# Performance work log

Hardware: AMD Instinct MI355X
Metric: run time of the kernel (lower is better)

The kernel has to match this reference:

```python
import jax, jax.numpy as jnp
import numpy as np
import math

B, T, D = 2, 2048, 1024
H, HD = 16, 64  # n_heads, head_dim; H*HD == D

def setup_inputs() -> dict:
    key = jax.random.key(0)
    ks = jax.random.split(key, 5)
    s = 1.0 / math.sqrt(D)
    return {
        "x": jax.random.normal(ks[0], (B, T, D), dtype=jnp.float32),
        "w_qkv": jax.random.normal(ks[1], (D, 3 * D), dtype=jnp.float32) * s,
        "b_qkv": jax.random.normal(ks[2], (3 * D,), dtype=jnp.float32) * 0.01,
        "w_o": jax.random.normal(ks[3], (D, D), dtype=jnp.float32) * s,
        "b_o": jax.random.normal(ks[4], (D,), dtype=jnp.float32) * 0.01,
    }

def reference(x, w_qkv, b_qkv, w_o, b_o):
    b, t, d_model = x.shape
    qkv = x @ w_qkv + b_qkv                       # [b,t,3d]
    q, k, v = jnp.split(qkv, 3, axis=-1)
    # [b,t,d] -> [b,h,t,hd]
    q = q.reshape(b, t, H, HD).transpose(0, 2, 1, 3)
    k = k.reshape(b, t, H, HD).transpose(0, 2, 1, 3)
    v = v.reshape(b, t, H, HD).transpose(0, 2, 1, 3)
    # NOTE: original scales by sqrt(d_model), not sqrt(head_dim)
    scores = jnp.einsum('bhqd,bhkd->bhqk', q, k) / math.sqrt(d_model)
    causal = jnp.tril(jnp.ones((t, t), dtype=bool))
    scores = jnp.where(causal[None, None], scores, -jnp.inf)
    # dropout p=0.0 (pre-softmax in original) is identity
    attn = jax.nn.softmax(scores, axis=-1)
    y = jnp.einsum('bhqk,bhkd->bhqd', attn, v)    # [b,h,t,hd]
    y = y.transpose(0, 2, 1, 3).reshape(b, t, d_model)
    return y @ w_o + b_o
```

## Files before the change

### kernel.cpp

```cpp
#include <hip/hip_runtime.h>
#include <math.h>

typedef __bf16 bf16;
typedef __bf16 bf16x4 __attribute__((ext_vector_type(4)));
typedef __bf16 bf16x8 __attribute__((ext_vector_type(8)));
typedef float f32x4 __attribute__((ext_vector_type(4)));

__device__ __forceinline__ void async_copy16(const void* g, void* l) {
  __builtin_amdgcn_global_load_lds(
      (__attribute__((address_space(1))) void*)(const_cast<void*>(g)),
      (__attribute__((address_space(3))) void*)(l),
      16, 0, 0);
}

__device__ __forceinline__ void transpose_tile(
    const float* __restrict__ in, bf16* __restrict__ out, int R, int C,
    int bxi, int byi) {
  __shared__ float tile[32][33];
  int bx = bxi * 32, by = byi * 32;
  int tx = threadIdx.x & 31;
  int ty = threadIdx.x >> 5;
#pragma unroll
  for (int i = 0; i < 32; i += 8)
    tile[ty + i][tx] = in[(size_t)(by + ty + i) * C + bx + tx];
  __syncthreads();
#pragma unroll
  for (int i = 0; i < 32; i += 8)
    out[(size_t)(bx + ty + i) * R + by + tx] = (bf16)tile[tx][ty + i];
}

__global__ __launch_bounds__(256) void prep_kernel(
    const float* __restrict__ x, bf16* __restrict__ xb,
    const float* __restrict__ w_qkv, bf16* __restrict__ wqkvT,
    const float* __restrict__ w_o, bf16* __restrict__ woT) {
  int blk = blockIdx.x;
  if (blk < 4096) {
    int i = blk * 1024 + threadIdx.x * 4;
    float4 v = *(const float4*)(x + i);
    bf16x4 o;
    o[0] = (bf16)v.x; o[1] = (bf16)v.y; o[2] = (bf16)v.z; o[3] = (bf16)v.w;
    *(bf16x4*)(xb + i) = o;
  } else if (blk < 7168) {
    int tb = blk - 4096;
    transpose_tile(w_qkv, wqkvT, 1024, 3072, tb % 96, tb / 96);
  } else {
    int tb = blk - 7168;
    transpose_tile(w_o, woT, 1024, 1024, tb % 32, tb / 32);
  }
}

__device__ __forceinline__ void gemm_mainloop(
    const bf16* __restrict__ A, const bf16* __restrict__ Bt, int K,
    int bm, int bn, bf16* As, bf16* Bs, f32x4 (&acc)[4][4]) {
  int tid = threadIdx.x;
  int w = tid >> 6, lane = tid & 63;
  int wm = w & 1, wn = w >> 1;
  int col = lane & 15, quad = lane >> 4;

  int srow = w * 32 + (lane >> 2);
  int scol = (lane & 3) * 8;
  const bf16* Ag0 = A + ((size_t)(bm * 128 + srow) * K + scol);
  const bf16* Bg0 = Bt + ((size_t)(bn * 128 + srow) * K + scol);
  bf16* AsW = As + (w * 32) * 32;
  bf16* BsW = Bs + (w * 32) * 32;

  for (int k0 = 0; k0 < K; k0 += 32) {
    __syncthreads();
    async_copy16(Ag0 + k0, AsW);
    async_copy16(Ag0 + k0 + (size_t)16 * K, AsW + 16 * 32);
    async_copy16(Bg0 + k0, BsW);
    async_copy16(Bg0 + k0 + (size_t)16 * K, BsW + 16 * 32);
    __syncthreads();

    bf16x8 af[4], bfr[4];
#pragma unroll
    for (int mi = 0; mi < 4; mi++)
      af[mi] = *(const bf16x8*)(As + (wm * 64 + mi * 16 + col) * 32 + quad * 8);
#pragma unroll
    for (int ni = 0; ni < 4; ni++)
      bfr[ni] = *(const bf16x8*)(Bs + (wn * 64 + ni * 16 + col) * 32 + quad * 8);
#pragma unroll
    for (int mi = 0; mi < 4; mi++)
#pragma unroll
      for (int ni = 0; ni < 4; ni++)
        acc[mi][ni] = __builtin_amdgcn_mfma_f32_16x16x32_bf16(
            af[mi], bfr[ni], acc[mi][ni], 0, 0, 0);
  }
}

__global__ __launch_bounds__(256) void gemm_qkv_kernel(
    const bf16* __restrict__ A, const bf16* __restrict__ Bt,
    const float* __restrict__ bias, bf16* __restrict__ qb,
    bf16* __restrict__ kb, bf16* __restrict__ vtb) {
  __shared__ bf16 As[128 * 32];
  __shared__ bf16 Bs[128 * 32];
  f32x4 acc[4][4] = {};
  int bm = blockIdx.x, bn = blockIdx.y;
  gemm_mainloop(A, Bt, 1024, bm, bn, As, Bs, acc);

  int tid = threadIdx.x;
  int w = tid >> 6, lane = tid & 63;
  int wm = w & 1, wn = w >> 1;
  int col = lane & 15, quad = lane >> 4;
#pragma unroll
  for (int ni = 0; ni < 4; ni++) {
    int gc = bn * 128 + wn * 64 + ni * 16 + col;
    float bv = bias[gc];
    int which = gc >> 10;
    int dd = gc & 1023;
    int h = dd >> 6, hd = dd & 63;
    if (which == 2) {
#pragma unroll
      for (int mi = 0; mi < 4; mi++) {
        int grow0 = bm * 128 + wm * 64 + mi * 16 + quad * 4;
        int b = grow0 >> 11, t0 = grow0 & 2047;
        bf16x4 pk;
#pragma unroll
        for (int r = 0; r < 4; r++) pk[r] = (bf16)(acc[mi][ni][r] + bv);
        *(bf16x4*)&vtb[(((size_t)(b * 16 + h) * 64 + hd) * 2048) + t0] = pk;
      }
    } else {
      bf16* dst = (which == 0) ? qb : kb;
#pragma unroll
      for (int mi = 0; mi < 4; mi++) {
#pragma unroll
        for (int r = 0; r < 4; r++) {
          int grow = bm * 128 + wm * 64 + mi * 16 + quad * 4 + r;
          int b = grow >> 11, t = grow & 2047;
          dst[(((size_t)(b * 16 + h) * 2048 + t) * 64) + hd] =
              (bf16)(acc[mi][ni][r] + bv);
        }
      }
    }
  }
}

__global__ __launch_bounds__(256) void gemm_out_kernel(
    const bf16* __restrict__ A, const bf16* __restrict__ Bt,
    const float* __restrict__ bias, float* __restrict__ outp) {
  __shared__ bf16 As[128 * 32];
  __shared__ bf16 Bs[128 * 32];
  f32x4 acc[4][4] = {};
  int bm = blockIdx.x, bn = blockIdx.y;
  gemm_mainloop(A, Bt, 1024, bm, bn, As, Bs, acc);

  int tid = threadIdx.x;
  int w = tid >> 6, lane = tid & 63;
  int wm = w & 1, wn = w >> 1;
  int col = lane & 15, quad = lane >> 4;
#pragma unroll
  for (int ni = 0; ni < 4; ni++) {
    int gc = bn * 128 + wn * 64 + ni * 16 + col;
    float bv = bias[gc];
#pragma unroll
    for (int mi = 0; mi < 4; mi++) {
#pragma unroll
      for (int r = 0; r < 4; r++) {
        int grow = bm * 128 + wm * 64 + mi * 16 + quad * 4 + r;
        outp[(size_t)grow * 1024 + gc] = acc[mi][ni][r] + bv;
      }
    }
  }
}

__global__ __launch_bounds__(256, 4) void attn_kernel(
    const bf16* __restrict__ qb, const bf16* __restrict__ kb,
    const bf16* __restrict__ vtb, bf16* __restrict__ y) {
  __shared__ bf16 Ks[64 * 64];
  __shared__ bf16 Vs[64 * 64];
  __shared__ bf16 Pl[4][16][72];

  int idx = blockIdx.x;
  int qt = 31 - (idx >> 5);
  int bh = idx & 31;
  int b = bh >> 4, h = bh & 15;
  int tid = threadIdx.x, w = tid >> 6, lane = tid & 63;
  int col = lane & 15, quad = lane >> 4;

  const bf16* Qh = qb + (size_t)bh * (2048 * 64);
  const bf16* Kh = kb + (size_t)bh * (2048 * 64);
  const bf16* Vth = vtb + (size_t)bh * (64 * 2048);

  int qrow = qt * 64 + w * 16 + col;
  bf16x8 aq[2];
#pragma unroll
  for (int ks = 0; ks < 2; ks++) {
    aq[ks] = *(const bf16x8*)(Qh + (size_t)qrow * 64 + ks * 32 + quad * 8);
#pragma unroll
    for (int e = 0; e < 8; e++)
      aq[ks][e] = (bf16)((float)aq[ks][e] * 0.03125f);
  }

  int r0 = w * 16 + (lane >> 3);
  int r1 = r0 + 8;
  int ch0 = (lane & 7) ^ (r0 & 7);
  int ch1 = (lane & 7) ^ (r1 & 7);
  size_t koff0 = (size_t)r0 * 64 + ch0 * 8;
  size_t koff1 = (size_t)r1 * 64 + ch1 * 8;
  size_t voff0 = (size_t)r0 * 2048 + ch0 * 8;
  size_t voff1 = (size_t)r1 * 2048 + ch1 * 8;
  bf16* KsW0 = Ks + (w * 16) * 64;
  bf16* KsW1 = Ks + (w * 16 + 8) * 64;
  bf16* VsW0 = Vs + (w * 16) * 64;
  bf16* VsW1 = Vs + (w * 16 + 8) * 64;

  float l_part = 0.f;
  f32x4 ot[4] = {};

  for (int j = 0; j <= qt; j++) {
    __syncthreads();
    {
      const bf16* Kt = Kh + (size_t)j * 64 * 64;
      const bf16* Vt_ = Vth + (size_t)j * 64;
      async_copy16(Kt + koff0, KsW0);
      async_copy16(Kt + koff1, KsW1);
      async_copy16(Vt_ + voff0, VsW0);
      async_copy16(Vt_ + voff1, VsW1);
    }
    __syncthreads();

    f32x4 st[4] = {};
#pragma unroll
    for (int ks = 0; ks < 2; ks++)
#pragma unroll
      for (int c = 0; c < 4; c++) {
        int t = c * 16 + col;
        int slot = t * 8 + (((ks << 2) + quad) ^ (t & 7));
        bf16x8 ak = *(const bf16x8*)(Ks + slot * 8);
        st[c] = __builtin_amdgcn_mfma_f32_16x16x32_bf16(ak, aq[ks], st[c],
                                                        0, 0, 0);
      }

    bool diag = (j == qt);
    int qglob = qt * 64 + w * 16 + col;
#pragma unroll
    for (int c = 0; c < 4; c++) {
      bf16x4 pk;
#pragma unroll
      for (int r = 0; r < 4; r++) {
        int tglob = j * 64 + c * 16 + quad * 4 + r;
        float pv = (diag && tglob > qglob) ? 0.f : __expf(st[c][r]);
        l_part += pv;
        pk[r] = (bf16)pv;
      }
      *(bf16x4*)&Pl[w][col][c * 16 + quad * 4] = pk;
    }

    __builtin_amdgcn_sched_barrier(0);
    __builtin_amdgcn_s_waitcnt(0xc07f);
    __builtin_amdgcn_sched_barrier(0);

    bf16x8 ap0 = *(const bf16x8*)&Pl[w][col][quad * 8];
    bf16x8 ap1 = *(const bf16x8*)&Pl[w][col][32 + quad * 8];
#pragma unroll
    for (int ks = 0; ks < 2; ks++)
#pragma unroll
      for (int c = 0; c < 4; c++) {
        int d = c * 16 + col;
        int slot = d * 8 + (((ks << 2) + quad) ^ (d & 7));
        bf16x8 av = *(const bf16x8*)(Vs + slot * 8);
        ot[c] = __builtin_amdgcn_mfma_f32_16x16x32_bf16(
            av, ks == 0 ? ap0 : ap1, ot[c], 0, 0, 0);
      }
  }

  float sum = l_part;
  sum += __shfl_xor(sum, 16, 64);
  sum += __shfl_xor(sum, 32, 64);
  float inv = 1.f / sum;
  int tq = qt * 64 + w * 16 + col;
  bf16* yrow = y + ((size_t)(b * 2048 + tq)) * 1024 + h * 64;
#pragma unroll
  for (int c = 0; c < 4; c++) {
    bf16x4 pk;
#pragma unroll
    for (int r = 0; r < 4; r++) pk[r] = (bf16)(ot[c][r] * inv);
    *(bf16x4*)(yrow + c * 16 + quad * 4) = pk;
  }
}

extern "C" void kernel_launch(void* const* d_in, const int* in_sizes, int n_in,
                              void* d_out, int out_size, void* d_ws,
                              size_t ws_size, hipStream_t stream) {
  const float* x = (const float*)d_in[0];
  const float* w_qkv = (const float*)d_in[1];
  const float* b_qkv = (const float*)d_in[2];
  const float* w_o = (const float*)d_in[3];
  const float* b_o = (const float*)d_in[4];
  float* out = (float*)d_out;

  char* p = (char*)d_ws;
  bf16* xb    = (bf16*)p; p += (size_t)4096 * 1024 * 2;
  bf16* wqkvT = (bf16*)p; p += (size_t)3072 * 1024 * 2;
  bf16* woT   = (bf16*)p; p += (size_t)1024 * 1024 * 2;
  bf16* qb    = (bf16*)p; p += (size_t)2 * 16 * 2048 * 64 * 2;
  bf16* kb    = (bf16*)p; p += (size_t)2 * 16 * 2048 * 64 * 2;
  bf16* vtb   = (bf16*)p; p += (size_t)2 * 16 * 64 * 2048 * 2;
  bf16* yb    = (bf16*)p; p += (size_t)4096 * 1024 * 2;

  prep_kernel<<<8192, 256, 0, stream>>>(x, xb, w_qkv, wqkvT, w_o, woT);
  gemm_qkv_kernel<<<dim3(32, 24), 256, 0, stream>>>(
      xb, wqkvT, b_qkv, qb, kb, vtb);
  attn_kernel<<<1024, 256, 0, stream>>>(qb, kb, vtb, yb);
  gemm_out_kernel<<<dim3(32, 8), 256, 0, stream>>>(yb, woT, b_o, out);
}
```

Before: 179.3 us.

## Load two KV tiles per barrier and rebalance causal q-tile scheduling

The attention loop now stages two K/V tiles into separate LDS buffers between each pair of barriers, halving the number of block-wide syncs and issuing more loads in flight. The P staging buffer is shrunk and the softmax/PV step is split into two halves, so each half's P values pass through LDS and feed the PV MFMA. Block-to-query-tile mapping is interleaved between long and short causal rows to even out per-CU work. This doubles K/V LDS usage, which may lower occupancy, and it still waits for both tiles before any compute starts, so there is no true overlap.

Result: faster. 169.9 us (-5.3%).

```diff
diff --git a/kernel.cpp b/kernel.cpp
--- a/kernel.cpp
+++ b/kernel.cpp
@@ -166,12 +166,16 @@
 __global__ __launch_bounds__(256, 4) void attn_kernel(
     const bf16* __restrict__ qb, const bf16* __restrict__ kb,
     const bf16* __restrict__ vtb, bf16* __restrict__ y) {
-  __shared__ bf16 Ks[64 * 64];
-  __shared__ bf16 Vs[64 * 64];
-  __shared__ bf16 Pl[4][16][72];
+  __shared__ bf16 Ks[2][64 * 64];
+  __shared__ bf16 Vs[2][64 * 64];
+  __shared__ bf16 Pl[4][16][40];
 
   int idx = blockIdx.x;
-  int qt = 31 - (idx >> 5);
+  int qp = idx >> 5;
+  int qt = (qp < 8) ? 31 - qp
+           : (qp < 16) ? qp - 8
+           : (qp < 24) ? 39 - qp
+                       : qp - 16;
   int bh = idx & 31;
   int b = bh >> 4, h = bh & 15;
   int tid = threadIdx.x, w = tid >> 6, lane = tid & 63;
@@ -199,26 +203,25 @@
   size_t koff1 = (size_t)r1 * 64 + ch1 * 8;
   size_t voff0 = (size_t)r0 * 2048 + ch0 * 8;
   size_t voff1 = (size_t)r1 * 2048 + ch1 * 8;
-  bf16* KsW0 = Ks + (w * 16) * 64;
-  bf16* KsW1 = Ks + (w * 16 + 8) * 64;
-  bf16* VsW0 = Vs + (w * 16) * 64;
-  bf16* VsW1 = Vs + (w * 16 + 8) * 64;
+  int lw0 = (w * 16) * 64;
+  int lw1 = (w * 16 + 8) * 64;
 
   float l_part = 0.f;
   f32x4 ot[4] = {};
-
-  for (int j = 0; j <= qt; j++) {
-    __syncthreads();
-    {
-      const bf16* Kt = Kh + (size_t)j * 64 * 64;
-      const bf16* Vt_ = Vth + (size_t)j * 64;
-      async_copy16(Kt + koff0, KsW0);
-      async_copy16(Kt + koff1, KsW1);
-      async_copy16(Vt_ + voff0, VsW0);
-      async_copy16(Vt_ + voff1, VsW1);
-    }
-    __syncthreads();
-
+  int qglob = qt * 64 + w * 16 + col;
+
+  auto stage = [&](int j, int buf) {
+    const bf16* Kt = Kh + (size_t)j * 64 * 64;
+    const bf16* Vt_ = Vth + (size_t)j * 64;
+    async_copy16(Kt + koff0, Ks[buf] + lw0);
+    async_copy16(Kt + koff1, Ks[buf] + lw1);
+    async_copy16(Vt_ + voff0, Vs[buf] + lw0);
+    async_copy16(Vt_ + voff1, Vs[buf] + lw1);
+  };
+
+  auto tile_compute = [&](int j, int buf, bool diag) {
+    const bf16* Ksb = Ks[buf];
+    const bf16* Vsb = Vs[buf];
     f32x4 st[4] = {};
 #pragma unroll
     for (int ks = 0; ks < 2; ks++)
@@ -226,42 +229,54 @@
       for (int c = 0; c < 4; c++) {
         int t = c * 16 + col;
         int slot = t * 8 + (((ks << 2) + quad) ^ (t & 7));
-        bf16x8 ak = *(const bf16x8*)(Ks + slot * 8);
+        bf16x8 ak = *(const bf16x8*)(Ksb + slot * 8);
         st[c] = __builtin_amdgcn_mfma_f32_16x16x32_bf16(ak, aq[ks], st[c],
                                                         0, 0, 0);
       }
-
-    bool diag = (j == qt);
-    int qglob = qt * 64 + w * 16 + col;
-#pragma unroll
-    for (int c = 0; c < 4; c++) {
-      bf16x4 pk;
-#pragma unroll
-      for (int r = 0; r < 4; r++) {
-        int tglob = j * 64 + c * 16 + quad * 4 + r;
-        float pv = (diag && tglob > qglob) ? 0.f : __expf(st[c][r]);
-        l_part += pv;
-        pk[r] = (bf16)pv;
-      }
-      *(bf16x4*)&Pl[w][col][c * 16 + quad * 4] = pk;
-    }
-
-    __builtin_amdgcn_sched_barrier(0);
-    __builtin_amdgcn_s_waitcnt(0xc07f);
-    __builtin_amdgcn_sched_barrier(0);
-
-    bf16x8 ap0 = *(const bf16x8*)&Pl[w][col][quad * 8];
-    bf16x8 ap1 = *(const bf16x8*)&Pl[w][col][32 + quad * 8];
-#pragma unroll
-    for (int ks = 0; ks < 2; ks++)
+#pragma unroll
+    for (int half = 0; half < 2; half++) {
+#pragma unroll
+      for (int cc = 0; cc < 2; cc++) {
+        int c = half * 2 + cc;
+        bf16x4 pk;
+#pragma unroll
+        for (int r = 0; r < 4; r++) {
+          int tglob = j * 64 + c * 16 + quad * 4 + r;
+          float pv = (diag && tglob > qglob) ? 0.f : __expf(st[c][r]);
+          l_part += pv;
+          pk[r] = (bf16)pv;
+        }
+        *(bf16x4*)&Pl[w][col][cc * 16 + quad * 4] = pk;
+      }
+      __builtin_amdgcn_sched_barrier(0);
+      __builtin_amdgcn_s_waitcnt(0xc07f);
+      __builtin_amdgcn_sched_barrier(0);
+      bf16x8 ap = *(const bf16x8*)&Pl[w][col][quad * 8];
 #pragma unroll
       for (int c = 0; c < 4; c++) {
         int d = c * 16 + col;
-        int slot = d * 8 + (((ks << 2) + quad) ^ (d & 7));
-        bf16x8 av = *(const bf16x8*)(Vs + slot * 8);
-        ot[c] = __builtin_amdgcn_mfma_f32_16x16x32_bf16(
-            av, ks == 0 ? ap0 : ap1, ot[c], 0, 0, 0);
-      }
+        int slot = d * 8 + (((half << 2) + quad) ^ (d & 7));
+        bf16x8 av = *(const bf16x8*)(Vsb + slot * 8);
+        ot[c] = __builtin_amdgcn_mfma_f32_16x16x32_bf16(av, ap, ot[c],
+                                                        0, 0, 0);
+      }
+    }
+  };
+
+  int j = 0;
+  for (; j < qt; j += 2) {
+    __syncthreads();
+    stage(j, 0);
+    stage(j + 1, 1);
+    __syncthreads();
+    tile_compute(j, 0, false);
+    tile_compute(j + 1, 1, j + 1 == qt);
+  }
+  if (j == qt) {
+    __syncthreads();
+    stage(j, 0);
+    __syncthreads();
+    tile_compute(j, 0, true);
   }
 
   float sum = l_part;
```
